# Kernel optimization log

Measured on AMD Instinct MI355X. Metric: run time of the kernel, lower is better.

Reference implementation:

```python
import jax, jax.numpy as jnp
import numpy as np

N_ROIS = 32768   # 8 images x 4096 proposals
N_GT = 1024      # 128 gt boxes / image
N_IMAGES = 8
N_CLASSES = 81   # COCO
FG_OVERLAP = 0.5


def _make_boxes(key, n, img_size=800.0, min_sz=16.0, max_sz=256.0):
    k1, k2, k3, k4 = jax.random.split(key, 4)
    x1 = jax.random.uniform(k1, (n,), minval=0.0, maxval=img_size - max_sz)
    y1 = jax.random.uniform(k2, (n,), minval=0.0, maxval=img_size - max_sz)
    w = jax.random.uniform(k3, (n,), minval=min_sz, maxval=max_sz)
    h = jax.random.uniform(k4, (n,), minval=min_sz, maxval=max_sz)
    return jnp.stack([x1, y1, x1 + w, y1 + h], axis=1)  # [n, 4]


def setup_inputs() -> dict:
    key = jax.random.key(0)
    kr, kg, kb1, kb2, kc, ks = jax.random.split(key, 6)
    roi_xy = _make_boxes(kr, N_ROIS)
    roi_score = jax.random.uniform(ks, (N_ROIS, 1))
    rois = jnp.concatenate([roi_xy, roi_score], axis=1)  # [N, 5]
    gt_xy = _make_boxes(kg, N_GT)
    gt_cls = jax.random.randint(kc, (N_GT, 1), 1, N_CLASSES).astype(jnp.float32)
    gt_boxes = jnp.concatenate([gt_xy, gt_cls], axis=1)  # [G, 5]
    roi_batch_inds = jax.random.randint(kb1, (N_ROIS,), 0, N_IMAGES)
    gt_batch_inds = jax.random.randint(kb2, (N_GT,), 0, N_IMAGES)
    return {"rois": rois, "roi_batch_inds": roi_batch_inds,
            "gt_boxes": gt_boxes, "gt_batch_inds": gt_batch_inds}


def _roi_target(rois4, gt4, gt_labels, same_batch):
    area_r = (rois4[:, 2] - rois4[:, 0] + 1.0) * (rois4[:, 3] - rois4[:, 1] + 1.0)  # [N]
    area_g = (gt4[:, 2] - gt4[:, 0] + 1.0) * (gt4[:, 3] - gt4[:, 1] + 1.0)          # [G]
    ix1 = jnp.maximum(rois4[:, None, 0], gt4[None, :, 0])
    iy1 = jnp.maximum(rois4[:, None, 1], gt4[None, :, 1])
    ix2 = jnp.minimum(rois4[:, None, 2], gt4[None, :, 2])
    iy2 = jnp.minimum(rois4[:, None, 3], gt4[None, :, 3])
    iw = jnp.clip(ix2 - ix1 + 1.0, 0.0)
    ih = jnp.clip(iy2 - iy1 + 1.0, 0.0)
    inter = iw * ih                                                     # [N, G]
    iou = inter / (area_r[:, None] + area_g[None, :] - inter)
    iou = jnp.where(same_batch, iou, -1.0)  # mask cross-image pairs

    best_gt = jnp.argmax(iou, axis=1)                # [N]
    max_ov = jnp.max(iou, axis=1)                    # [N]
    fg = max_ov >= FG_OVERLAP                        # [N]

    labels = jnp.where(fg, gt_labels[best_gt].astype(jnp.int32), 0)

    g = gt4[best_gt]  # matched gt box per roi, [N, 4]
    ew = rois4[:, 2] - rois4[:, 0] + 1.0
    eh = rois4[:, 3] - rois4[:, 1] + 1.0
    ecx = rois4[:, 0] + 0.5 * ew
    ecy = rois4[:, 1] + 0.5 * eh
    gw = g[:, 2] - g[:, 0] + 1.0
    gh = g[:, 3] - g[:, 1] + 1.0
    gcx = g[:, 0] + 0.5 * gw
    gcy = g[:, 1] + 0.5 * gh
    deltas = jnp.stack([(gcx - ecx) / ew,
                        (gcy - ecy) / eh,
                        jnp.log(gw / ew),
                        jnp.log(gh / eh)], axis=1)   # [N, 4]
    fg4 = fg[:, None]
    deltas = jnp.where(fg4, deltas, 0.0)
    bbwgts = jnp.where(fg4, 1.0, 0.0)
    return labels, deltas, bbwgts


def reference(rois, roi_batch_inds, gt_boxes, gt_batch_inds):
    rois4 = rois[:, :4]
    gt4 = gt_boxes[:, :4]
    gt_labels = gt_boxes[:, 4]
    same_batch = roi_batch_inds[:, None] == gt_batch_inds[None, :]  # [N, G]
    return _roi_target(rois4, gt4, gt_labels, same_batch)
```

## Files before the change

kernel.cpp:

```cpp
#include <hip/hip_runtime.h>

#define N_ROIS 32768
#define N_GT   1024
#define N_IMG  8
#define CHUNKS 16
#define MBLOCK 512
#define MGRID  256
#define ROIS_PER_PASS (MBLOCK / CHUNKS)
#define ROIS_PER_BLOCK (N_ROIS / MGRID)
#define PASSES (ROIS_PER_BLOCK / ROIS_PER_PASS)

#define WS_BOX  0
#define WS_AREA 4096
#define WS_OJ   5120
#define WS_SEG  6144

__global__ __launch_bounds__(256) void gt_sort_kernel(
    const float* __restrict__ gt_boxes,
    const int*   __restrict__ gt_b,
    float*       __restrict__ ws)
{
    __shared__ int s_chist[16][N_IMG];
    __shared__ int s_cbase[16][N_IMG];

    int tid  = threadIdx.x;
    int lane = tid & 63;
    int wave = tid >> 6;

    unsigned long long lt_mask = (lane == 63) ? (~0ull >> 1)
                                              : ((1ull << lane) - 1ull);

    int   bv[4];
    float bx1[4], by1[4], bx2[4], by2[4];
    #pragma unroll
    for (int k = 0; k < 4; ++k) {
        int j = (wave * 4 + k) * 64 + lane;
        bv[k]  = gt_b[j];
        bx1[k] = gt_boxes[j * 5 + 0];
        by1[k] = gt_boxes[j * 5 + 1];
        bx2[k] = gt_boxes[j * 5 + 2];
        by2[k] = gt_boxes[j * 5 + 3];
    }

    int rankc[4];
    #pragma unroll
    for (int k = 0; k < 4; ++k) {
        int b = bv[k];
        unsigned long long mym = 0;
        #pragma unroll
        for (int bb = 0; bb < N_IMG; ++bb) {
            unsigned long long m = __ballot(b == bb);
            if (b == bb) mym = m;
            if (lane == bb) s_chist[wave * 4 + k][bb] = __popcll(m);
        }
        rankc[k] = __popcll(mym & lt_mask);
    }
    __syncthreads();

    if (wave == 0) {
        int myc    = lane & 15;
        int myb_lo = lane >> 4;
        int myb_hi = myb_lo + 4;
        int cnt_lo = s_chist[myc][myb_lo];
        int cnt_hi = s_chist[myc][myb_hi];
        int inc_lo = cnt_lo, inc_hi = cnt_hi;
        #pragma unroll
        for (int d = 1; d < 16; d <<= 1) {
            int t_lo = __shfl_up(inc_lo, d, 16);
            int t_hi = __shfl_up(inc_hi, d, 16);
            if (myc >= d) { inc_lo += t_lo; inc_hi += t_hi; }
        }
        int t0 = __shfl(inc_lo, 15, 64);
        int t1 = __shfl(inc_lo, 31, 64);
        int t2 = __shfl(inc_lo, 47, 64);
        int t3 = __shfl(inc_lo, 63, 64);
        int t4 = __shfl(inc_hi, 15, 64);
        int t5 = __shfl(inc_hi, 31, 64);
        int t6 = __shfl(inc_hi, 47, 64);
        int t7 = __shfl(inc_hi, 63, 64);

        int s0 = 0;
        int s1 = s0 + t0, s2 = s1 + t1, s3 = s2 + t2, s4 = s3 + t3;
        int s5 = s4 + t4, s6 = s5 + t5, s7 = s6 + t6, s8 = s7 + t7;

        if (lane == 0) {
            int* wseg = (int*)(ws + WS_SEG);
            wseg[0] = s0; wseg[1] = s1; wseg[2] = s2; wseg[3] = s3;
            wseg[4] = s4; wseg[5] = s5; wseg[6] = s6; wseg[7] = s7;
            wseg[8] = s8;
        }
        int seg_lo = (myb_lo == 0) ? s0 : (myb_lo == 1) ? s1
                   : (myb_lo == 2) ? s2 : s3;
        int seg_hi = (myb_hi == 4) ? s4 : (myb_hi == 5) ? s5
                   : (myb_hi == 6) ? s6 : s7;
        s_cbase[myc][myb_lo] = seg_lo + (inc_lo - cnt_lo);
        s_cbase[myc][myb_hi] = seg_hi + (inc_hi - cnt_hi);
    }
    __syncthreads();

    float4* wbox  = (float4*)(ws + WS_BOX);
    float*  warea = ws + WS_AREA;
    int*    woj   = (int*)(ws + WS_OJ);
    #pragma unroll
    for (int k = 0; k < 4; ++k) {
        int chunk = wave * 4 + k;
        int j     = chunk * 64 + lane;
        int rank  = s_cbase[chunk][bv[k]] + rankc[k];
        wbox[rank]  = make_float4(bx1[k], by1[k], bx2[k], by2[k]);
        warea[rank] = __fmul_rn(__fadd_rn(__fsub_rn(bx2[k], bx1[k]), 1.0f),
                                __fadd_rn(__fsub_rn(by2[k], by1[k]), 1.0f));
        woj[rank]   = j;
    }
}

__global__ __launch_bounds__(MBLOCK) void roi_target_kernel(
    const float* __restrict__ rois,
    const int*   __restrict__ roi_b,
    const float* __restrict__ gt_boxes,
    const float* __restrict__ ws,
    float*       __restrict__ out)
{
    __shared__ float4 s_box[N_GT];
    __shared__ float  s_area[N_GT];
    __shared__ int    s_oj[N_GT];
    __shared__ int    s_seg[N_IMG + 1];

    const float4* wbox  = (const float4*)(ws + WS_BOX);
    const float*  warea = ws + WS_AREA;
    const int*    woj   = (const int*)(ws + WS_OJ);
    const int*    wseg  = (const int*)(ws + WS_SEG);

    for (int t = threadIdx.x; t < N_GT; t += MBLOCK) {
        s_box[t]  = wbox[t];
        s_area[t] = warea[t];
        s_oj[t]   = woj[t];
    }
    if (threadIdx.x <= N_IMG) s_seg[threadIdx.x] = wseg[threadIdx.x];
    __syncthreads();

    int c = threadIdx.x & (CHUNKS - 1);

    #pragma unroll
    for (int pass = 0; pass < PASSES; ++pass) {
        int roi = blockIdx.x * ROIS_PER_BLOCK + pass * ROIS_PER_PASS
                + (threadIdx.x >> 4);

        float rx1 = rois[roi * 5 + 0];
        float ry1 = rois[roi * 5 + 1];
        float rx2 = rois[roi * 5 + 2];
        float ry2 = rois[roi * 5 + 3];
        int   rb  = roi_b[roi];
        float area_r = __fmul_rn(__fadd_rn(__fsub_rn(rx2, rx1), 1.0f),
                                 __fadd_rn(__fsub_rn(ry2, ry1), 1.0f));

        int st = s_seg[rb];
        int en = s_seg[rb + 1];

        float best = -2.0f;
        int   bp   = -1;
        for (int p = st + c; p < en; p += CHUNKS) {
            float4 b  = s_box[p];
            float ix1 = fmaxf(rx1, b.x);
            float iy1 = fmaxf(ry1, b.y);
            float ix2 = fminf(rx2, b.z);
            float iy2 = fminf(ry2, b.w);
            float iw  = fmaxf(__fadd_rn(__fsub_rn(ix2, ix1), 1.0f), 0.0f);
            float ih  = fmaxf(__fadd_rn(__fsub_rn(iy2, iy1), 1.0f), 0.0f);
            float inter = __fmul_rn(iw, ih);
            float uni = __fsub_rn(__fadd_rn(area_r, s_area[p]), inter);
            float v   = __fdiv_rn(inter, uni);
            if (v > best) { best = v; bp = p; }
        }

        #pragma unroll
        for (int m = 1; m < CHUNKS; m <<= 1) {
            float vo = __shfl_xor(best, m, 64);
            int   po = __shfl_xor(bp,   m, 64);
            if (vo > best || (vo == best && po < bp)) { best = vo; bp = po; }
        }

        if (c == 0) {
            bool fg = (best >= 0.5f);
            int  pp = (bp < 0) ? 0 : bp;

            float label = 0.0f;
            if (fg) label = gt_boxes[s_oj[pp] * 5 + 4];

            float4 g  = s_box[pp];
            float ew  = __fadd_rn(__fsub_rn(rx2, rx1), 1.0f);
            float eh  = __fadd_rn(__fsub_rn(ry2, ry1), 1.0f);
            float ecx = __fadd_rn(rx1, __fmul_rn(0.5f, ew));
            float ecy = __fadd_rn(ry1, __fmul_rn(0.5f, eh));
            float gw  = __fadd_rn(__fsub_rn(g.z, g.x), 1.0f);
            float gh  = __fadd_rn(__fsub_rn(g.w, g.y), 1.0f);
            float gcx = __fadd_rn(g.x, __fmul_rn(0.5f, gw));
            float gcy = __fadd_rn(g.y, __fmul_rn(0.5f, gh));

            float dx = __fdiv_rn(__fsub_rn(gcx, ecx), ew);
            float dy = __fdiv_rn(__fsub_rn(gcy, ecy), eh);
            float dw = logf(__fdiv_rn(gw, ew));
            float dh = logf(__fdiv_rn(gh, eh));

            if (!fg) { dx = 0.0f; dy = 0.0f; dw = 0.0f; dh = 0.0f; }
            float wgt = fg ? 1.0f : 0.0f;

            out[roi] = label;
            float4* dout = (float4*)(out + N_ROIS) + roi;
            *dout = make_float4(dx, dy, dw, dh);
            float4* wout = (float4*)(out + N_ROIS + 4 * N_ROIS) + roi;
            *wout = make_float4(wgt, wgt, wgt, wgt);
        }
    }
}

extern "C" void kernel_launch(void* const* d_in, const int* in_sizes, int n_in,
                              void* d_out, int out_size, void* d_ws, size_t ws_size,
                              hipStream_t stream) {
    const float* rois  = (const float*)d_in[0];
    const int*   roi_b = (const int*)d_in[1];
    const float* gt    = (const float*)d_in[2];
    const int*   gt_b  = (const int*)d_in[3];
    float*       ws    = (float*)d_ws;
    float*       out   = (float*)d_out;

    gt_sort_kernel<<<1, 256, 0, stream>>>(gt, gt_b, ws);
    roi_target_kernel<<<MGRID, MBLOCK, 0, stream>>>(rois, roi_b, gt, ws, out);
}
```

Before: 73.11 us.

## Fuse GT bucket-sort into the ROI target kernel, drop workspace round trip

Each of the 256 blocks now redundantly counting-sorts the 1024 GT boxes by image directly into shared memory. This removes the separate single-block sort kernel launch and the global workspace write/read between the two kernels. GT labels are also kept in shared memory instead of being gathered from global memory through an index array. The cost is that every block repeats the sort work (ballots, scan, global loads of all GT boxes) before starting its IoU loop.

```diff
diff --git a/kernel.cpp b/kernel.cpp
--- a/kernel.cpp
+++ b/kernel.cpp
@@ -9,19 +9,22 @@
 #define ROIS_PER_PASS (MBLOCK / CHUNKS)
 #define ROIS_PER_BLOCK (N_ROIS / MGRID)
 #define PASSES (ROIS_PER_BLOCK / ROIS_PER_PASS)
-
-#define WS_BOX  0
-#define WS_AREA 4096
-#define WS_OJ   5120
-#define WS_SEG  6144
-
-__global__ __launch_bounds__(256) void gt_sort_kernel(
+#define GT_CHUNKS 16
+#define CHUNKS_PER_WAVE 2
+
+__global__ __launch_bounds__(MBLOCK) void roi_target_kernel(
+    const float* __restrict__ rois,
+    const int*   __restrict__ roi_b,
     const float* __restrict__ gt_boxes,
     const int*   __restrict__ gt_b,
-    float*       __restrict__ ws)
+    float*       __restrict__ out)
 {
-    __shared__ int s_chist[16][N_IMG];
-    __shared__ int s_cbase[16][N_IMG];
+    __shared__ float4 s_box[N_GT];
+    __shared__ float  s_area[N_GT];
+    __shared__ float  s_lab[N_GT];
+    __shared__ int    s_chist[GT_CHUNKS][N_IMG];
+    __shared__ int    s_cbase[GT_CHUNKS][N_IMG];
+    __shared__ int    s_seg[N_IMG + 1];
 
     int tid  = threadIdx.x;
     int lane = tid & 63;
@@ -30,28 +33,30 @@
     unsigned long long lt_mask = (lane == 63) ? (~0ull >> 1)
                                               : ((1ull << lane) - 1ull);
 
-    int   bv[4];
-    float bx1[4], by1[4], bx2[4], by2[4];
-    #pragma unroll
-    for (int k = 0; k < 4; ++k) {
-        int j = (wave * 4 + k) * 64 + lane;
-        bv[k]  = gt_b[j];
-        bx1[k] = gt_boxes[j * 5 + 0];
-        by1[k] = gt_boxes[j * 5 + 1];
-        bx2[k] = gt_boxes[j * 5 + 2];
-        by2[k] = gt_boxes[j * 5 + 3];
-    }
-
-    int rankc[4];
-    #pragma unroll
-    for (int k = 0; k < 4; ++k) {
+    int   bv[CHUNKS_PER_WAVE];
+    float bx1[CHUNKS_PER_WAVE], by1[CHUNKS_PER_WAVE];
+    float bx2[CHUNKS_PER_WAVE], by2[CHUNKS_PER_WAVE], blab[CHUNKS_PER_WAVE];
+    #pragma unroll
+    for (int k = 0; k < CHUNKS_PER_WAVE; ++k) {
+        int j = (wave * CHUNKS_PER_WAVE + k) * 64 + lane;
+        bv[k]   = gt_b[j];
+        bx1[k]  = gt_boxes[j * 5 + 0];
+        by1[k]  = gt_boxes[j * 5 + 1];
+        bx2[k]  = gt_boxes[j * 5 + 2];
+        by2[k]  = gt_boxes[j * 5 + 3];
+        blab[k] = gt_boxes[j * 5 + 4];
+    }
+
+    int rankc[CHUNKS_PER_WAVE];
+    #pragma unroll
+    for (int k = 0; k < CHUNKS_PER_WAVE; ++k) {
         int b = bv[k];
         unsigned long long mym = 0;
         #pragma unroll
         for (int bb = 0; bb < N_IMG; ++bb) {
             unsigned long long m = __ballot(b == bb);
             if (b == bb) mym = m;
-            if (lane == bb) s_chist[wave * 4 + k][bb] = __popcll(m);
+            if (lane == bb) s_chist[wave * CHUNKS_PER_WAVE + k][bb] = __popcll(m);
         }
         rankc[k] = __popcll(mym & lt_mask);
     }
@@ -84,10 +89,9 @@
         int s5 = s4 + t4, s6 = s5 + t5, s7 = s6 + t6, s8 = s7 + t7;
 
         if (lane == 0) {
-            int* wseg = (int*)(ws + WS_SEG);
-            wseg[0] = s0; wseg[1] = s1; wseg[2] = s2; wseg[3] = s3;
-            wseg[4] = s4; wseg[5] = s5; wseg[6] = s6; wseg[7] = s7;
-            wseg[8] = s8;
+            s_seg[0] = s0; s_seg[1] = s1; s_seg[2] = s2; s_seg[3] = s3;
+            s_seg[4] = s4; s_seg[5] = s5; s_seg[6] = s6; s_seg[7] = s7;
+            s_seg[8] = s8;
         }
         int seg_lo = (myb_lo == 0) ? s0 : (myb_lo == 1) ? s1
                    : (myb_lo == 2) ? s2 : s3;
@@ -98,52 +102,23 @@
     }
     __syncthreads();
 
-    float4* wbox  = (float4*)(ws + WS_BOX);
-    float*  warea = ws + WS_AREA;
-    int*    woj   = (int*)(ws + WS_OJ);
-    #pragma unroll
-    for (int k = 0; k < 4; ++k) {
-        int chunk = wave * 4 + k;
-        int j     = chunk * 64 + lane;
+    #pragma unroll
+    for (int k = 0; k < CHUNKS_PER_WAVE; ++k) {
+        int chunk = wave * CHUNKS_PER_WAVE + k;
         int rank  = s_cbase[chunk][bv[k]] + rankc[k];
-        wbox[rank]  = make_float4(bx1[k], by1[k], bx2[k], by2[k]);
-        warea[rank] = __fmul_rn(__fadd_rn(__fsub_rn(bx2[k], bx1[k]), 1.0f),
-                                __fadd_rn(__fsub_rn(by2[k], by1[k]), 1.0f));
-        woj[rank]   = j;
-    }
-}
-
-__global__ __launch_bounds__(MBLOCK) void roi_target_kernel(
-    const float* __restrict__ rois,
-    const int*   __restrict__ roi_b,
-    const float* __restrict__ gt_boxes,
-    const float* __restrict__ ws,
-    float*       __restrict__ out)
-{
-    __shared__ float4 s_box[N_GT];
-    __shared__ float  s_area[N_GT];
-    __shared__ int    s_oj[N_GT];
-    __shared__ int    s_seg[N_IMG + 1];
-
-    const float4* wbox  = (const float4*)(ws + WS_BOX);
-    const float*  warea = ws + WS_AREA;
-    const int*    woj   = (const int*)(ws + WS_OJ);
-    const int*    wseg  = (const int*)(ws + WS_SEG);
-
-    for (int t = threadIdx.x; t < N_GT; t += MBLOCK) {
-        s_box[t]  = wbox[t];
-        s_area[t] = warea[t];
-        s_oj[t]   = woj[t];
-    }
-    if (threadIdx.x <= N_IMG) s_seg[threadIdx.x] = wseg[threadIdx.x];
+        s_box[rank]  = make_float4(bx1[k], by1[k], bx2[k], by2[k]);
+        s_area[rank] = __fmul_rn(__fadd_rn(__fsub_rn(bx2[k], bx1[k]), 1.0f),
+                                 __fadd_rn(__fsub_rn(by2[k], by1[k]), 1.0f));
+        s_lab[rank]  = blab[k];
+    }
     __syncthreads();
 
-    int c = threadIdx.x & (CHUNKS - 1);
+    int c = tid & (CHUNKS - 1);
 
     #pragma unroll
     for (int pass = 0; pass < PASSES; ++pass) {
         int roi = blockIdx.x * ROIS_PER_BLOCK + pass * ROIS_PER_PASS
-                + (threadIdx.x >> 4);
+                + (tid >> 4);
 
         float rx1 = rois[roi * 5 + 0];
         float ry1 = rois[roi * 5 + 1];
@@ -183,8 +158,7 @@
             bool fg = (best >= 0.5f);
             int  pp = (bp < 0) ? 0 : bp;
 
-            float label = 0.0f;
-            if (fg) label = gt_boxes[s_oj[pp] * 5 + 4];
+            float label = fg ? s_lab[pp] : 0.0f;
 
             float4 g  = s_box[pp];
             float ew  = __fadd_rn(__fsub_rn(rx2, rx1), 1.0f);
@@ -220,9 +194,7 @@
     const int*   roi_b = (const int*)d_in[1];
     const float* gt    = (const float*)d_in[2];
     const int*   gt_b  = (const int*)d_in[3];
-    float*       ws    = (float*)d_ws;
     float*       out   = (float*)d_out;
 
-    gt_sort_kernel<<<1, 256, 0, stream>>>(gt, gt_b, ws);
-    roi_target_kernel<<<MGRID, MBLOCK, 0, stream>>>(rois, roi_b, gt, ws, out);
+    roi_target_kernel<<<MGRID, MBLOCK, 0, stream>>>(rois, roi_b, gt, gt_b, out);
 }
```

After: 70.13 us. -4.1%, faster.
